# Kernel optimization log

Measured on AMD Instinct MI355X. Metric: run time of the kernel, lower is better.

The kernel has to match this reference:

```python
import jax, jax.numpy as jnp
import numpy as np

EMBED = 768
HEADS = 12
HEAD_DIM = EMBED // HEADS
FFN = 4 * EMBED
EPS = 1e-5


def setup_inputs() -> dict:
    key = jax.random.key(0)
    ks = jax.random.split(key, 12)
    s = 0.02
    inp = {
        'x': jax.random.normal(ks[0], (1, 4096, EMBED), dtype=jnp.float32),
        'Wq': jax.random.normal(ks[1], (EMBED, EMBED), dtype=jnp.float32) * s,
        'bq': jnp.zeros((EMBED,), jnp.float32),
        'Wk': jax.random.normal(ks[2], (EMBED, EMBED), dtype=jnp.float32) * s,
        'bk': jnp.zeros((EMBED,), jnp.float32),
        'Wv': jax.random.normal(ks[3], (EMBED, EMBED), dtype=jnp.float32) * s,
        'bv': jnp.zeros((EMBED,), jnp.float32),
        'Wo': jax.random.normal(ks[4], (EMBED, EMBED), dtype=jnp.float32) * s,
        'bo': jnp.zeros((EMBED,), jnp.float32),
        'ln1_g': jnp.ones((EMBED,), jnp.float32),
        'ln1_b': jnp.zeros((EMBED,), jnp.float32),
        'W1': jax.random.normal(ks[5], (EMBED, FFN), dtype=jnp.float32) * s,
        'b1': jnp.zeros((FFN,), jnp.float32),
        'W2': jax.random.normal(ks[6], (FFN, EMBED), dtype=jnp.float32) * s,
        'b2': jnp.zeros((EMBED,), jnp.float32),
        'ln2_g': jnp.ones((EMBED,), jnp.float32),
        'ln2_b': jnp.zeros((EMBED,), jnp.float32),
    }
    return inp


def _layernorm(x, g, b):
    mu = jnp.mean(x, axis=-1, keepdims=True)
    var = jnp.mean(jnp.square(x - mu), axis=-1, keepdims=True)
    return (x - mu) * jax.lax.rsqrt(var + EPS) * g + b


def reference(x, Wq, bq, Wk, bk, Wv, bv, Wo, bo, ln1_g, ln1_b, W1, b1, W2, b2, ln2_g, ln2_b):
    B, S, D = x.shape
    # QKV projections -> [B, H, S, d]
    def split_heads(t):
        return t.reshape(B, S, HEADS, HEAD_DIM).transpose(0, 2, 1, 3)
    q = split_heads(x @ Wq + bq)
    k = split_heads(x @ Wk + bk)
    v = split_heads(x @ Wv + bv)
    scores = jnp.einsum('bhqd,bhkd->bhqk', q, k) / np.sqrt(HEAD_DIM).astype(np.float32)
    attn = jax.nn.softmax(scores, axis=-1)
    ctx = jnp.einsum('bhqk,bhkd->bhqd', attn, v)
    ctx = ctx.transpose(0, 2, 1, 3).reshape(B, S, D)
    attn_out = ctx @ Wo + bo
    h = _layernorm(x + attn_out, ln1_g, ln1_b)
    ffn = jax.nn.gelu(h @ W1 + b1, approximate=False) @ W2 + b2
    return _layernorm(h + ffn, ln2_g, ln2_b)
```

## Files before the change

kernel.cpp:

```cpp
#include <hip/hip_runtime.h>
#include <hip/hip_bf16.h>

typedef __attribute__((ext_vector_type(8))) short s16x8;
typedef __attribute__((ext_vector_type(4))) int   i32x4;
typedef __attribute__((ext_vector_type(4))) float f32x4;
typedef __attribute__((ext_vector_type(8))) __bf16 bf16x8;

__device__ __forceinline__ short f2bf(float f) {
  unsigned u = __builtin_bit_cast(unsigned, f);
  u = (u + 0x7FFFu + ((u >> 16) & 1u)) >> 16;
  return (short)u;
}
__device__ __forceinline__ float bf2f(short s) {
  unsigned u = ((unsigned)(unsigned short)s) << 16;
  return __builtin_bit_cast(float, u);
}
__device__ __forceinline__ f32x4 mfma16(s16x8 a, s16x8 b, f32x4 c) {
  return __builtin_amdgcn_mfma_f32_16x16x32_bf16(
      __builtin_bit_cast(bf16x8, a), __builtin_bit_cast(bf16x8, b), c, 0, 0, 0);
}
__device__ __forceinline__ void gload16(const void* g, void* l) {
  __builtin_amdgcn_global_load_lds(
      (const __attribute__((address_space(1))) void*)g,
      (__attribute__((address_space(3))) void*)l, 16, 0, 0);
}

__global__ __launch_bounds__(256) void convert_x_kernel(const float* __restrict__ src,
                                                        short* __restrict__ dst, int n8) {
  int i = blockIdx.x * 256 + threadIdx.x;
  if (i >= n8) return;
  float4 v0 = ((const float4*)src)[i * 2];
  float4 v1 = ((const float4*)src)[i * 2 + 1];
  s16x8 o;
  o[0] = f2bf(v0.x); o[1] = f2bf(v0.y); o[2] = f2bf(v0.z); o[3] = f2bf(v0.w);
  o[4] = f2bf(v1.x); o[5] = f2bf(v1.y); o[6] = f2bf(v1.z); o[7] = f2bf(v1.w);
  *(s16x8*)&dst[i * 8] = o;
}

__global__ __launch_bounds__(256) void bconcat_kernel(const float* __restrict__ bq,
                                                      const float* __restrict__ bk,
                                                      const float* __restrict__ bv,
                                                      float* __restrict__ out) {
  int i = blockIdx.x * 256 + threadIdx.x;
  if (i < 2304) out[i] = i < 768 ? bq[i] : (i < 1536 ? bk[i - 768] : bv[i - 1536]);
}

__global__ __launch_bounds__(256) void wconv_kernel(const float* __restrict__ src,
                                                    short* __restrict__ dst, int K, int N) {
  __shared__ float t[32][33];
  int n0 = blockIdx.x * 32, k0 = blockIdx.y * 32;
  int tx = threadIdx.x & 31, ty = threadIdx.x >> 5;
#pragma unroll
  for (int r = 0; r < 4; ++r) t[ty + r * 8][tx] = src[(long)(k0 + ty + r * 8) * N + n0 + tx];
  __syncthreads();
#pragma unroll
  for (int r = 0; r < 4; ++r)
    dst[(long)(n0 + ty + r * 8) * K + k0 + tx] = f2bf(t[tx][ty + r * 8]);
}

__global__ __launch_bounds__(256) void vtrans_kernel(const short* __restrict__ qkv,
                                                     short* __restrict__ vt) {
  __shared__ short t[32][34];
  int c0 = blockIdx.x * 32, s0 = blockIdx.y * 32;
  int tx = threadIdx.x & 31, ty = threadIdx.x >> 5;
#pragma unroll
  for (int r = 0; r < 4; ++r)
    t[ty + r * 8][tx] = qkv[(long)(s0 + ty + r * 8) * 2304 + 1536 + c0 + tx];
  __syncthreads();
#pragma unroll
  for (int r = 0; r < 4; ++r)
    vt[(long)(c0 + ty + r * 8) * 4096 + s0 + tx] = t[tx][ty + r * 8];
}

template <int OUT_MODE>
__global__ __launch_bounds__(256) void gemm_kernel(const short* __restrict__ A,
                                                   const short* __restrict__ Bt,
                                                   const float* __restrict__ bias,
                                                   void* __restrict__ Cout,
                                                   int M, int N, int Kfull, int Ksub) {
  __shared__ short As[2][128 * 32];
  __shared__ short Bs[2][128 * 32];
  const int tid = threadIdx.x;
  const int wave = tid >> 6, lane = tid & 63;
  const int lr = lane & 15, lg = lane >> 4;
  const int wm = wave >> 1, wn = wave & 1;
  const int bm = blockIdx.x, bn = blockIdx.y;
  const long koff = (long)blockIdx.z * Ksub;

  f32x4 acc[4][4] = {};

  const int r0 = tid >> 2;
  const int cc = (tid & 3) * 8;
  const short* Ag0 = A + (long)(bm * 128 + r0) * Kfull + koff + cc;
  const short* Ag1 = Ag0 + (long)64 * Kfull;
  const short* Bg0 = Bt + (long)(bn * 128 + r0) * Kfull + koff + cc;
  const short* Bg1 = Bg0 + (long)64 * Kfull;

  auto STAGE = [&](int buf, int k0) {
    gload16(Ag0 + k0, &As[buf][tid * 8]);
    gload16(Ag1 + k0, &As[buf][64 * 32 + tid * 8]);
    gload16(Bg0 + k0, &Bs[buf][tid * 8]);
    gload16(Bg1 + k0, &Bs[buf][64 * 32 + tid * 8]);
  };
  auto COMPUTE = [&](int buf) {
    s16x8 af[4], bfr[4];
#pragma unroll
    for (int m = 0; m < 4; ++m) {
      int row = wm * 64 + m * 16 + lr;
      af[m] = *(const s16x8*)&As[buf][row * 32 + lg * 8];
    }
#pragma unroll
    for (int n = 0; n < 4; ++n) {
      int row = wn * 64 + n * 16 + lr;
      bfr[n] = *(const s16x8*)&Bs[buf][row * 32 + lg * 8];
    }
#pragma unroll
    for (int m = 0; m < 4; ++m)
#pragma unroll
      for (int n = 0; n < 4; ++n)
        acc[m][n] = mfma16(af[m], bfr[n], acc[m][n]);
  };

  const int nt = Ksub >> 5;
  STAGE(0, 0);
  int cur = 0;
  for (int t = 0; t < nt - 1; ++t) {
    STAGE(cur ^ 1, (t + 1) * 32);
    asm volatile("s_waitcnt vmcnt(4)" ::: "memory");
    __builtin_amdgcn_s_barrier();
    __builtin_amdgcn_sched_barrier(0);
    COMPUTE(cur);
    __builtin_amdgcn_s_barrier();
    cur ^= 1;
  }
  asm volatile("s_waitcnt vmcnt(0)" ::: "memory");
  __builtin_amdgcn_s_barrier();
  __builtin_amdgcn_sched_barrier(0);
  COMPUTE(cur);

  const int gr0 = bm * 128 + wm * 64 + lg * 4;
  const int gc0 = bn * 128 + wn * 64 + lr;
  float* outF = (float*)Cout + (long)blockIdx.z * M * N;
#pragma unroll
  for (int n = 0; n < 4; ++n) {
    int col = gc0 + n * 16;
    float bb = (blockIdx.z == 0) ? bias[col] : 0.f;
#pragma unroll
    for (int m = 0; m < 4; ++m) {
#pragma unroll
      for (int j = 0; j < 4; ++j) {
        int row = gr0 + m * 16 + j;
        float v = acc[m][n][j] + bb;
        if (OUT_MODE == 2) v = 0.5f * v * (1.0f + erff(v * 0.70710678118f));
        if (OUT_MODE == 1) outF[(long)row * N + col] = v;
        else ((short*)Cout)[(long)row * N + col] = f2bf(v);
      }
    }
  }
}

__global__ __launch_bounds__(256) void flash_kernel(const short* __restrict__ qkv,
                                                    const short* __restrict__ vt,
                                                    float* __restrict__ Opart,
                                                    float* __restrict__ Lpart) {
  __shared__ short Kt[64 * 64];
  __shared__ short Vs[64 * 64];
  __shared__ short Ps[128 * 72];
  const int tid = threadIdx.x;
  const int wave = tid >> 6, lane = tid & 63;
  const int lr = lane & 15, lg = lane >> 4;
  const int lb = blockIdx.x + 32 * blockIdx.y + 384 * blockIdx.z;
  const int nlb = (lb & 7) * 96 + (lb >> 3);
  const int qb = nlb & 31;
  const int h = (nlb >> 5) % 12;
  const int sp = nlb / 384;
  const int qc = h * 64;
  const int hc = 768 + h * 64;
  const int vr = h * 64;
  const float QSCALE = 0.125f * 1.44269504088896f;

  i32x4 kr[2], vrg[2];
  auto LOADREGS = [&](int s0) {
#pragma unroll
    for (int i = 0; i < 2; ++i) {
      int c = tid + i * 256, row = c >> 3, ch = c & 7;
      kr[i] = *(const i32x4*)&qkv[(long)(s0 + row) * 2304 + hc + ch * 8];
      vrg[i] = *(const i32x4*)&vt[(long)(vr + row) * 4096 + s0 + ch * 8];
    }
  };
  auto WRITELDS = [&]() {
#pragma unroll
    for (int i = 0; i < 2; ++i) {
      int c = tid + i * 256, row = c >> 3, ch = c & 7;
      int sc = ch ^ (row & 7);
      *(i32x4*)&Kt[row * 64 + sc * 8] = kr[i];
      *(i32x4*)&Vs[row * 64 + sc * 8] = vrg[i];
    }
  };

  LOADREGS(sp * 2048);

#pragma unroll
  for (int i = 0; i < 4; ++i) {
    int c = tid + i * 256;
    int row = c >> 3, cq = (c & 7) * 8;
    *(i32x4*)&Ps[row * 72 + cq] =
        *(const i32x4*)&qkv[(long)(qb * 128 + row) * 2304 + qc + cq];
  }
  __syncthreads();
  s16x8 qf[2][2];
#pragma unroll
  for (int m = 0; m < 2; ++m)
#pragma unroll
    for (int ks = 0; ks < 2; ++ks) {
      int row = wave * 32 + m * 16 + lr;
      s16x8 v = *(const s16x8*)&Ps[row * 72 + ks * 32 + lg * 8];
#pragma unroll
      for (int e = 0; e < 8; ++e) {
        __bf16 b = (__bf16)(bf2f(v[e]) * QSCALE);
        v[e] = (short)__builtin_bit_cast(unsigned short, b);
      }
      qf[m][ks] = v;
    }

  float l_part[8];
#pragma unroll
  for (int i = 0; i < 8; ++i) l_part[i] = 0.f;
  f32x4 oacc[2][4] = {};

  for (int it = 0; it < 32; ++it) {
    WRITELDS();
    if (it != 31) LOADREGS(sp * 2048 + (it + 1) * 64);
    asm volatile("s_waitcnt lgkmcnt(0)" ::: "memory");
    __builtin_amdgcn_s_barrier();
    __builtin_amdgcn_sched_barrier(0);

    f32x4 sacc[2][4] = {};
#pragma unroll
    for (int ks = 0; ks < 2; ++ks) {
      s16x8 kf[4];
#pragma unroll
      for (int n = 0; n < 4; ++n) {
        int row = n * 16 + lr;
        int chk = (ks * 4 + lg) ^ (lr & 7);
        kf[n] = *(const s16x8*)&Kt[row * 64 + chk * 8];
      }
      __builtin_amdgcn_s_setprio(1);
#pragma unroll
      for (int m = 0; m < 2; ++m)
#pragma unroll
        for (int n = 0; n < 4; ++n)
          sacc[m][n] = mfma16(qf[m][ks], kf[n], sacc[m][n]);
      __builtin_amdgcn_s_setprio(0);
    }
#pragma unroll
    for (int m = 0; m < 2; ++m) {
#pragma unroll
      for (int j = 0; j < 4; ++j) {
        const int prow = wave * 32 + m * 16 + lg * 4 + j;
        float rs = 0.f;
#pragma unroll
        for (int n = 0; n < 4; ++n) {
          float p = __builtin_amdgcn_exp2f(sacc[m][n][j]);
          rs += p;
          ((__bf16*)Ps)[prow * 72 + n * 16 + lr] = (__bf16)p;
        }
        l_part[m * 4 + j] += rs;
      }
    }
#pragma unroll
    for (int ks = 0; ks < 2; ++ks) {
      s16x8 pf[2], vf[4];
#pragma unroll
      for (int m = 0; m < 2; ++m) {
        int row = wave * 32 + m * 16 + lr;
        pf[m] = *(const s16x8*)&Ps[row * 72 + ks * 32 + lg * 8];
      }
#pragma unroll
      for (int n = 0; n < 4; ++n) {
        int row = n * 16 + lr;
        int chk = (ks * 4 + lg) ^ (lr & 7);
        vf[n] = *(const s16x8*)&Vs[row * 64 + chk * 8];
      }
      __builtin_amdgcn_s_setprio(1);
#pragma unroll
      for (int m = 0; m < 2; ++m)
#pragma unroll
        for (int n = 0; n < 4; ++n)
          oacc[m][n] = mfma16(pf[m], vf[n], oacc[m][n]);
      __builtin_amdgcn_s_setprio(0);
    }
    __builtin_amdgcn_s_barrier();
  }

  const long pbase = ((long)(h * 32 + qb) * 2 + sp) * 128;
#pragma unroll
  for (int m = 0; m < 2; ++m)
#pragma unroll
    for (int j = 0; j < 4; ++j) {
      float l = l_part[m * 4 + j];
      l += __shfl_xor(l, 1);
      l += __shfl_xor(l, 2);
      l += __shfl_xor(l, 4);
      l += __shfl_xor(l, 8);
      if (lr == 0) Lpart[pbase + wave * 32 + m * 16 + lg * 4 + j] = l;
    }
#pragma unroll
  for (int m = 0; m < 2; ++m)
#pragma unroll
    for (int n = 0; n < 4; ++n)
#pragma unroll
      for (int j = 0; j < 4; ++j) {
        int row = wave * 32 + m * 16 + lg * 4 + j;
        Opart[(pbase + row) * 64 + n * 16 + lr] = oacc[m][n][j];
      }
}

__global__ __launch_bounds__(256) void combine_kernel(const float* __restrict__ Opart,
                                                      const float* __restrict__ Lpart,
                                                      short* __restrict__ ctx) {
  const int row = blockIdx.x;
  const int col = blockIdx.y * 256 + threadIdx.x;
  const int h = col >> 6, c = col & 63;
  const int qb = row >> 7, r = row & 127;
  const long p0 = ((long)(h * 32 + qb) * 2) * 128 + r;
  const long p1 = p0 + 128;
  float l = Lpart[p0] + Lpart[p1];
  float o = Opart[p0 * 64 + c] + Opart[p1 * 64 + c];
  ctx[(long)row * 768 + col] = f2bf(o / l);
}

__global__ __launch_bounds__(256) void ln_kernel(const float* __restrict__ a,
                                                 const float* __restrict__ b,
                                                 const float* __restrict__ c,
                                                 const float* __restrict__ g,
                                                 const float* __restrict__ be,
                                                 float* __restrict__ of,
                                                 short* __restrict__ ob) {
  const int row = blockIdx.x;
  const int tid = threadIdx.x;
  const long base = (long)row * 768;
  float v[3];
  float s1 = 0.f, s2 = 0.f;
#pragma unroll
  for (int kk = 0; kk < 3; ++kk) {
    int i = tid + kk * 256;
    float x = a[base + i] + b[base + i] + c[base + i];
    v[kk] = x;
    s1 += x;
    s2 += x * x;
  }
#pragma unroll
  for (int off = 1; off < 64; off <<= 1) {
    s1 += __shfl_xor(s1, off);
    s2 += __shfl_xor(s2, off);
  }
  __shared__ float ws1[4], ws2[4];
  int wave = tid >> 6;
  if ((tid & 63) == 0) { ws1[wave] = s1; ws2[wave] = s2; }
  __syncthreads();
  s1 = ws1[0] + ws1[1] + ws1[2] + ws1[3];
  s2 = ws2[0] + ws2[1] + ws2[2] + ws2[3];
  float mean = s1 * (1.f / 768.f);
  float var = s2 * (1.f / 768.f) - mean * mean;
  float rstd = rsqrtf(var + 1e-5f);
#pragma unroll
  for (int kk = 0; kk < 3; ++kk) {
    int i = tid + kk * 256;
    float o = (v[kk] - mean) * rstd * g[i] + be[i];
    if (of) of[base + i] = o;
    if (ob) ob[base + i] = f2bf(o);
  }
}

extern "C" void kernel_launch(void* const* d_in, const int* in_sizes, int n_in,
                              void* d_out, int out_size, void* d_ws, size_t ws_size,
                              hipStream_t stream) {
  const float* x   = (const float*)d_in[0];
  const float* Wq  = (const float*)d_in[1];
  const float* bq  = (const float*)d_in[2];
  const float* Wk  = (const float*)d_in[3];
  const float* bk  = (const float*)d_in[4];
  const float* Wv  = (const float*)d_in[5];
  const float* bv  = (const float*)d_in[6];
  const float* Wo  = (const float*)d_in[7];
  const float* bo  = (const float*)d_in[8];
  const float* g1  = (const float*)d_in[9];
  const float* be1 = (const float*)d_in[10];
  const float* W1  = (const float*)d_in[11];
  const float* b1  = (const float*)d_in[12];
  const float* W2  = (const float*)d_in[13];
  const float* b2  = (const float*)d_in[14];
  const float* g2  = (const float*)d_in[15];
  const float* be2 = (const float*)d_in[16];

  char* ws = (char*)d_ws;
  size_t off = 0;
  auto alloc = [&](size_t bytes) {
    char* p = ws + off;
    off += (bytes + 255) & ~(size_t)255;
    return p;
  };
  short* xb     = (short*)alloc(4096ul * 768 * 2);
  short* wqkv_t = (short*)alloc(2304ul * 768 * 2);
  short* wo_t   = (short*)alloc(768ul * 768 * 2);
  short* w1_t   = (short*)alloc(3072ul * 768 * 2);
  short* w2_t   = (short*)alloc(768ul * 3072 * 2);
  float* bqkv   = (float*)alloc(2304ul * 4);
  short* qkv    = (short*)alloc(4096ul * 2304 * 2);
  short* vt     = (short*)alloc(768ul * 4096 * 2);
  short* ctx    = (short*)alloc(4096ul * 768 * 2);
  float* attn_o = (float*)alloc(4096ul * 768 * 4);
  short* h_b    = (short*)alloc(4096ul * 768 * 2);
  float* h_f    = (float*)alloc(4096ul * 768 * 4);
  short* f1     = (short*)alloc(4096ul * 3072 * 2);
  float* Opart  = (float*)f1;
  float* Lpart  = (float*)attn_o;
  float* attn_p = (float*)qkv;
  float* ffn_p  = (float*)qkv;

  convert_x_kernel<<<1536, 256, 0, stream>>>(x, xb, 4096 * 768 / 8);
  bconcat_kernel<<<9, 256, 0, stream>>>(bq, bk, bv, bqkv);
  wconv_kernel<<<dim3(24, 24), 256, 0, stream>>>(Wq, wqkv_t, 768, 768);
  wconv_kernel<<<dim3(24, 24), 256, 0, stream>>>(Wk, wqkv_t + 768 * 768, 768, 768);
  wconv_kernel<<<dim3(24, 24), 256, 0, stream>>>(Wv, wqkv_t + 2 * 768 * 768, 768, 768);
  wconv_kernel<<<dim3(24, 24), 256, 0, stream>>>(Wo, wo_t, 768, 768);
  wconv_kernel<<<dim3(96, 24), 256, 0, stream>>>(W1, w1_t, 768, 3072);
  wconv_kernel<<<dim3(24, 96), 256, 0, stream>>>(W2, w2_t, 3072, 768);

  gemm_kernel<0><<<dim3(32, 18), 256, 0, stream>>>(xb, wqkv_t, bqkv, qkv, 4096, 2304, 768, 768);
  vtrans_kernel<<<dim3(24, 128), 256, 0, stream>>>(qkv, vt);
  flash_kernel<<<dim3(32, 12, 2), 256, 0, stream>>>(qkv, vt, Opart, Lpart);
  combine_kernel<<<dim3(4096, 3), 256, 0, stream>>>(Opart, Lpart, ctx);
  gemm_kernel<1><<<dim3(32, 6, 2), 256, 0, stream>>>(ctx, wo_t, bo, attn_p, 4096, 768, 768, 384);
  ln_kernel<<<4096, 256, 0, stream>>>(x, attn_p, attn_p + 4096ul * 768, g1, be1, h_f, h_b);
  gemm_kernel<2><<<dim3(32, 24), 256, 0, stream>>>(h_b, w1_t, b1, f1, 4096, 3072, 768, 768);
  gemm_kernel<1><<<dim3(32, 6, 2), 256, 0, stream>>>(f1, w2_t, b2, ffn_p, 4096, 768, 3072, 1536);
  ln_kernel<<<4096, 256, 0, stream>>>(h_f, ffn_p, ffn_p + 4096ul * 768, g2, be2, (float*)d_out, nullptr);
}
```

Measured before the change: 255.0 us.

## Double-buffer K/V LDS tiles and transpose S MFMA for packed P stores

The flash attention kernel now keeps two K/V shared-memory buffers, so the next tile is written into the alternate buffer after the PV step. This leaves one barrier per iteration instead of two. The QK^T MFMA swaps its operands so each lane holds four consecutive key scores for one query row. That lets P be stored as packed 4-wide bf16 vectors and the row-sum reduction shrink to two shuffles. The cost is doubled K/V LDS use, which may reduce occupancy.

```diff
diff --git a/kernel.cpp b/kernel.cpp
--- a/kernel.cpp
+++ b/kernel.cpp
@@ -5,6 +5,7 @@
 typedef __attribute__((ext_vector_type(4))) int   i32x4;
 typedef __attribute__((ext_vector_type(4))) float f32x4;
 typedef __attribute__((ext_vector_type(8))) __bf16 bf16x8;
+typedef __attribute__((ext_vector_type(4))) __bf16 bf16x4;
 
 __device__ __forceinline__ short f2bf(float f) {
   unsigned u = __builtin_bit_cast(unsigned, f);
@@ -163,8 +164,8 @@
                                                     const short* __restrict__ vt,
                                                     float* __restrict__ Opart,
                                                     float* __restrict__ Lpart) {
-  __shared__ short Kt[64 * 64];
-  __shared__ short Vs[64 * 64];
+  __shared__ short Kt[2][64 * 64];
+  __shared__ short Vs[2][64 * 64];
   __shared__ short Ps[128 * 72];
   const int tid = threadIdx.x;
   const int wave = tid >> 6, lane = tid & 63;
@@ -188,17 +189,18 @@
       vrg[i] = *(const i32x4*)&vt[(long)(vr + row) * 4096 + s0 + ch * 8];
     }
   };
-  auto WRITELDS = [&]() {
+  auto WRITELDS = [&](int buf) {
 #pragma unroll
     for (int i = 0; i < 2; ++i) {
       int c = tid + i * 256, row = c >> 3, ch = c & 7;
       int sc = ch ^ (row & 7);
-      *(i32x4*)&Kt[row * 64 + sc * 8] = kr[i];
-      *(i32x4*)&Vs[row * 64 + sc * 8] = vrg[i];
+      *(i32x4*)&Kt[buf][row * 64 + sc * 8] = kr[i];
+      *(i32x4*)&Vs[buf][row * 64 + sc * 8] = vrg[i];
     }
   };
 
-  LOADREGS(sp * 2048);
+  const int sbase = sp * 2048;
+  LOADREGS(sbase);
 
 #pragma unroll
   for (int i = 0; i < 4; ++i) {
@@ -207,7 +209,13 @@
     *(i32x4*)&Ps[row * 72 + cq] =
         *(const i32x4*)&qkv[(long)(qb * 128 + row) * 2304 + qc + cq];
   }
-  __syncthreads();
+  asm volatile("s_waitcnt vmcnt(0)" ::: "memory");
+  WRITELDS(0);
+  LOADREGS(sbase + 64);
+  asm volatile("s_waitcnt lgkmcnt(0)" ::: "memory");
+  __builtin_amdgcn_s_barrier();
+  __builtin_amdgcn_sched_barrier(0);
+
   s16x8 qf[2][2];
 #pragma unroll
   for (int m = 0; m < 2; ++m)
@@ -223,18 +231,11 @@
       qf[m][ks] = v;
     }
 
-  float l_part[8];
-#pragma unroll
-  for (int i = 0; i < 8; ++i) l_part[i] = 0.f;
+  float l_part[2] = {0.f, 0.f};
   f32x4 oacc[2][4] = {};
 
+  int cur = 0;
   for (int it = 0; it < 32; ++it) {
-    WRITELDS();
-    if (it != 31) LOADREGS(sp * 2048 + (it + 1) * 64);
-    asm volatile("s_waitcnt lgkmcnt(0)" ::: "memory");
-    __builtin_amdgcn_s_barrier();
-    __builtin_amdgcn_sched_barrier(0);
-
     f32x4 sacc[2][4] = {};
 #pragma unroll
     for (int ks = 0; ks < 2; ++ks) {
@@ -243,30 +244,33 @@
       for (int n = 0; n < 4; ++n) {
         int row = n * 16 + lr;
         int chk = (ks * 4 + lg) ^ (lr & 7);
-        kf[n] = *(const s16x8*)&Kt[row * 64 + chk * 8];
+        kf[n] = *(const s16x8*)&Kt[cur][row * 64 + chk * 8];
       }
       __builtin_amdgcn_s_setprio(1);
 #pragma unroll
       for (int m = 0; m < 2; ++m)
 #pragma unroll
         for (int n = 0; n < 4; ++n)
-          sacc[m][n] = mfma16(qf[m][ks], kf[n], sacc[m][n]);
+          sacc[m][n] = mfma16(kf[n], qf[m][ks], sacc[m][n]);
       __builtin_amdgcn_s_setprio(0);
     }
 #pragma unroll
     for (int m = 0; m < 2; ++m) {
-#pragma unroll
-      for (int j = 0; j < 4; ++j) {
-        const int prow = wave * 32 + m * 16 + lg * 4 + j;
-        float rs = 0.f;
-#pragma unroll
-        for (int n = 0; n < 4; ++n) {
-          float p = __builtin_amdgcn_exp2f(sacc[m][n][j]);
-          rs += p;
-          ((__bf16*)Ps)[prow * 72 + n * 16 + lr] = (__bf16)p;
-        }
-        l_part[m * 4 + j] += rs;
-      }
+      const int prow = wave * 32 + m * 16 + lr;
+      float rs = 0.f;
+#pragma unroll
+      for (int n = 0; n < 4; ++n) {
+        float p0 = __builtin_amdgcn_exp2f(sacc[m][n][0]);
+        float p1 = __builtin_amdgcn_exp2f(sacc[m][n][1]);
+        float p2 = __builtin_amdgcn_exp2f(sacc[m][n][2]);
+        float p3 = __builtin_amdgcn_exp2f(sacc[m][n][3]);
+        rs += (p0 + p1) + (p2 + p3);
+        bf16x4 pk;
+        pk[0] = (__bf16)p0; pk[1] = (__bf16)p1;
+        pk[2] = (__bf16)p2; pk[3] = (__bf16)p3;
+        *(bf16x4*)&Ps[prow * 72 + n * 16 + lg * 4] = pk;
+      }
+      l_part[m] += rs;
     }
 #pragma unroll
     for (int ks = 0; ks < 2; ++ks) {
@@ -280,7 +284,7 @@
       for (int n = 0; n < 4; ++n) {
         int row = n * 16 + lr;
         int chk = (ks * 4 + lg) ^ (lr & 7);
-        vf[n] = *(const s16x8*)&Vs[row * 64 + chk * 8];
+        vf[n] = *(const s16x8*)&Vs[cur][row * 64 + chk * 8];
       }
       __builtin_amdgcn_s_setprio(1);
 #pragma unroll
@@ -290,21 +294,25 @@
           oacc[m][n] = mfma16(pf[m], vf[n], oacc[m][n]);
       __builtin_amdgcn_s_setprio(0);
     }
-    __builtin_amdgcn_s_barrier();
+    if (it < 31) {
+      asm volatile("s_waitcnt vmcnt(0)" ::: "memory");
+      WRITELDS(cur ^ 1);
+      if (it < 30) LOADREGS(sbase + (it + 2) * 64);
+      asm volatile("s_waitcnt lgkmcnt(0)" ::: "memory");
+      __builtin_amdgcn_s_barrier();
+      __builtin_amdgcn_sched_barrier(0);
+      cur ^= 1;
+    }
   }
 
   const long pbase = ((long)(h * 32 + qb) * 2 + sp) * 128;
 #pragma unroll
-  for (int m = 0; m < 2; ++m)
-#pragma unroll
-    for (int j = 0; j < 4; ++j) {
-      float l = l_part[m * 4 + j];
-      l += __shfl_xor(l, 1);
-      l += __shfl_xor(l, 2);
-      l += __shfl_xor(l, 4);
-      l += __shfl_xor(l, 8);
-      if (lr == 0) Lpart[pbase + wave * 32 + m * 16 + lg * 4 + j] = l;
-    }
+  for (int m = 0; m < 2; ++m) {
+    float l = l_part[m];
+    l += __shfl_xor(l, 16);
+    l += __shfl_xor(l, 32);
+    if (lane < 16) Lpart[pbase + wave * 32 + m * 16 + lr] = l;
+  }
 #pragma unroll
   for (int m = 0; m < 2; ++m)
 #pragma unroll
```

Result: faster. 241.3 us (-5.4%).
